# Kernel tuning notes

Hardware: AMD Instinct MI355X
Metric: run time of the kernel (lower is better)

The kernel has to match this reference:

```python
import jax, jax.numpy as jnp
import numpy as np

D, K = 512, 32


def setup_inputs() -> dict:
    key = jax.random.key(0)
    k1, k2, k3 = jax.random.split(key, 3)
    X = jax.random.normal(k1, (8, D, 128, 128), dtype=jnp.float32)
    std1 = 1.0 / (K * D) ** 0.5
    codewords = jax.random.uniform(k2, (K, D), dtype=jnp.float32, minval=-std1, maxval=std1)
    scale = jax.random.uniform(k3, (K,), dtype=jnp.float32, minval=-1.0, maxval=0.0)
    return {"X": X, "codewords": codewords, "scale": scale}


def reference(X, codewords, scale):
    B = X.shape[0]
    # [B, D, H, W] -> [B, N, D]
    Xf = X.reshape(B, D, -1).transpose(0, 2, 1)
    # scaled L2: s_k * ||x_i - d_k||^2, expanded to avoid [B,N,K,D] residuals
    x2 = jnp.sum(Xf * Xf, axis=-1, keepdims=True)            # [B, N, 1]
    c2 = jnp.sum(codewords * codewords, axis=-1)              # [K]
    xc = jnp.einsum('bnd,kd->bnk', Xf, codewords)             # [B, N, K]
    sl = scale * (x2 - 2.0 * xc + c2)                         # [B, N, K]
    A = jax.nn.softmax(sl, axis=2)                            # [B, N, K]
    # E[b,k,d] = sum_n A[b,n,k] * (X[b,n,d] - C[k,d])
    E = jnp.einsum('bnk,bnd->bkd', A, Xf) - jnp.sum(A, axis=1)[..., None] * codewords
    return E
```

## Files before the change

### kernel.cpp

```cpp
#include <hip/hip_runtime.h>
#include <stdint.h>

#define B_ 8
#define D_ 512
#define N_ 16384
#define K_ 32

typedef __attribute__((ext_vector_type(8))) short short8;
typedef __attribute__((ext_vector_type(16))) float f32x16;

union F8 { short8 v; unsigned short s[8]; uint32_t u[4]; uint4 q; };

__device__ __forceinline__ uint32_t bfpack2(float lo, float hi) {
    uint32_t a = __float_as_uint(lo);
    uint32_t b = __float_as_uint(hi);
    a += 0x7FFFu + ((a >> 16) & 1u);
    b += 0x7FFFu + ((b >> 16) & 1u);
    return (a >> 16) | (b & 0xFFFF0000u);
}
__device__ __forceinline__ unsigned short bf16of(float x) {
    uint32_t a = __float_as_uint(x);
    a += 0x7FFFu + ((a >> 16) & 1u);
    return (unsigned short)(a >> 16);
}
__device__ __forceinline__ float bflo(uint32_t v) { return __uint_as_float(v << 16); }
__device__ __forceinline__ float bfhi(uint32_t v) { return __uint_as_float(v & 0xFFFF0000u); }

__device__ __forceinline__ void bar_lds() {
    __builtin_amdgcn_s_waitcnt(0xC07F);
    __builtin_amdgcn_s_barrier();
}

__launch_bounds__(512, 4)
__global__ void encode_kernel(const float* __restrict__ X,
                              const float* __restrict__ Cg,
                              const float* __restrict__ scale,
                              float* __restrict__ part,
                              float* __restrict__ aSumAcc)
{
    __shared__ uint32_t xsTw[D_ * 20];
    __shared__ unsigned short lgpS[8 * 32 * 40];
    __shared__ uint32_t A_ldsw[K_ * 20];
    __shared__ float    x2p[8][32];
    __shared__ float    scs[K_], c2s[K_];
    __shared__ float    c2tmp[K_][17];
    __shared__ float    aSumLds[K_];

    unsigned short* xsTs  = (unsigned short*)xsTw;
    unsigned short* A_lds = (unsigned short*)A_ldsw;

    const int tid = threadIdx.x;
    const int l   = tid & 63;
    const int w   = __builtin_amdgcn_readfirstlane(tid >> 6);
    const int lc  = l & 31;
    const int nh  = l >> 5;
    const int b     = blockIdx.x >> 6;
    const int chunk = blockIdx.x & 63;

    {
        int k = tid >> 4, dg = tid & 15;
        const float* cr = Cg + k * D_ + dg * 32;
        float s2 = 0.f;
#pragma unroll
        for (int i = 0; i < 8; ++i) {
            float4 v = *(const float4*)(cr + i * 4);
            s2 += v.x * v.x + v.y * v.y + v.z * v.z + v.w * v.w;
        }
        c2tmp[k][dg] = s2;
        if (tid < K_) { scs[tid] = scale[tid]; aSumLds[tid] = 0.f; }
    }
    __syncthreads();
    if (tid < K_) {
        float s = 0.f;
#pragma unroll
        for (int dg = 0; dg < 16; ++dg) s += c2tmp[tid][dg];
        c2s[tid] = s;
    }

    F8 cfr[4];
#pragma unroll
    for (int ss = 0; ss < 4; ++ss) {
        int d0 = 64 * w + ss * 16 + nh * 8;
        const float* cp = Cg + lc * D_ + d0;
        float4 a  = *(const float4*)(cp);
        float4 bq = *(const float4*)(cp + 4);
        cfr[ss].u[0] = bfpack2(a.x, a.y);
        cfr[ss].u[1] = bfpack2(a.z, a.w);
        cfr[ss].u[2] = bfpack2(bq.x, bq.y);
        cfr[ss].u[3] = bfpack2(bq.z, bq.w);
    }

    f32x16 eacc[2];
#pragma unroll
    for (int ti = 0; ti < 2; ++ti)
#pragma unroll
        for (int r = 0; r < 16; ++r) eacc[ti][r] = 0.f;
    float aSumReg[4] = {0.f, 0.f, 0.f, 0.f};

    const int nl  = l >> 3;
    const int kq  = l & 7;
    const int smn = (w & 3) * 8 + nl;
    const int k0  = kq * 4;

    const int dl = tid >> 3;
    const int nq = tid & 7;
    const size_t xbase = (size_t)b * D_ * N_ + (size_t)chunk * 256;

    for (int t = 0; t < 8; ++t) {
        bar_lds();

        {
            const float* Xp = X + xbase + t * 32 + nq * 4;
            float4 x2a; x2a.x = x2a.y = x2a.z = x2a.w = 0.f;
#pragma unroll
            for (int r = 0; r < 8; ++r) {
                int d = dl + 64 * r;
                float4 v = *(const float4*)(Xp + (size_t)d * N_);
                x2a.x += v.x * v.x; x2a.y += v.y * v.y;
                x2a.z += v.z * v.z; x2a.w += v.w * v.w;
                uint2 p;
                p.x = bfpack2(v.x, v.y);
                p.y = bfpack2(v.z, v.w);
                *(uint2*)&xsTw[d * 20 + nq * 2] = p;
            }
#pragma unroll
            for (int m = 8; m <= 32; m <<= 1) {
                x2a.x += __shfl_xor(x2a.x, m);
                x2a.y += __shfl_xor(x2a.y, m);
                x2a.z += __shfl_xor(x2a.z, m);
                x2a.w += __shfl_xor(x2a.w, m);
            }
            if (l < 8) *(float4*)&x2p[w][nq * 4] = x2a;
        }

        bar_lds();

        {
            f32x16 lacc;
#pragma unroll
            for (int r = 0; r < 16; ++r) lacc[r] = 0.f;
#pragma unroll
            for (int ss = 0; ss < 4; ++ss) {
                int d0 = 64 * w + ss * 16 + nh * 8;
                F8 af;
#pragma unroll
                for (int j = 0; j < 8; ++j)
                    af.s[j] = xsTs[(d0 + j) * 40 + lc];
                lacc = __builtin_amdgcn_mfma_f32_32x32x16_bf16(af.v, cfr[ss].v, lacc, 0, 0, 0);
            }
#pragma unroll
            for (int r = 0; r < 16; ++r) {
                int row = (r & 3) + 8 * (r >> 2) + 4 * nh;
                lgpS[(w * 32 + row) * 40 + lc] = bf16of(lacc[r]);
            }
        }

        bar_lds();

        if (w < 4) {
            float xc0 = 0.f, xc1 = 0.f, xc2 = 0.f, xc3 = 0.f;
#pragma unroll
            for (int wp = 0; wp < 8; ++wp) {
                uint2 pv = *(const uint2*)&lgpS[(wp * 32 + smn) * 40 + k0];
                xc0 += bflo(pv.x); xc1 += bfhi(pv.x);
                xc2 += bflo(pv.y); xc3 += bfhi(pv.y);
            }
            float x2v = 0.f;
#pragma unroll
            for (int wp = 0; wp < 8; ++wp) x2v += x2p[wp][smn];
            float sl0 = scs[k0]     * (x2v - 2.f * xc0 + c2s[k0]);
            float sl1 = scs[k0 + 1] * (x2v - 2.f * xc1 + c2s[k0 + 1]);
            float sl2 = scs[k0 + 2] * (x2v - 2.f * xc2 + c2s[k0 + 2]);
            float sl3 = scs[k0 + 3] * (x2v - 2.f * xc3 + c2s[k0 + 3]);
            float m = fmaxf(fmaxf(sl0, sl1), fmaxf(sl2, sl3));
#pragma unroll
            for (int mk = 1; mk <= 4; mk <<= 1) m = fmaxf(m, __shfl_xor(m, mk));
            float e0 = __expf(sl0 - m), e1 = __expf(sl1 - m);
            float e2 = __expf(sl2 - m), e3 = __expf(sl3 - m);
            float s = e0 + e1 + e2 + e3;
#pragma unroll
            for (int mk = 1; mk <= 4; mk <<= 1) s += __shfl_xor(s, mk);
            float inv = 1.f / s;
            e0 *= inv; e1 *= inv; e2 *= inv; e3 *= inv;
            aSumReg[0] += e0; aSumReg[1] += e1;
            aSumReg[2] += e2; aSumReg[3] += e3;
            A_lds[(k0)     * 40 + smn] = bf16of(e0);
            A_lds[(k0 + 1) * 40 + smn] = bf16of(e1);
            A_lds[(k0 + 2) * 40 + smn] = bf16of(e2);
            A_lds[(k0 + 3) * 40 + smn] = bf16of(e3);
        }

        bar_lds();

#pragma unroll
        for (int ti = 0; ti < 2; ++ti) {
            int dcol = 64 * w + 32 * ti + lc;
#pragma unroll
            for (int ns = 0; ns < 2; ++ns) {
                F8 af, bf;
                af.q = *(const uint4*)&A_lds[lc * 40 + ns * 16 + nh * 8];
                bf.q = *(const uint4*)&xsTs[dcol * 40 + ns * 16 + nh * 8];
                eacc[ti] = __builtin_amdgcn_mfma_f32_32x32x16_bf16(af.v, bf.v, eacc[ti], 0, 0, 0);
            }
        }
    }

    float* pB = part + (size_t)blockIdx.x * (K_ * D_);
#pragma unroll
    for (int ti = 0; ti < 2; ++ti) {
        int d = 64 * w + 32 * ti + lc;
#pragma unroll
        for (int r = 0; r < 16; ++r) {
            int k = (r & 3) + 8 * (r >> 2) + 4 * nh;
            pB[k * D_ + d] = eacc[ti][r];
        }
    }

    if (w < 4) {
#pragma unroll
        for (int i = 0; i < 4; ++i) {
#pragma unroll
            for (int m = 8; m <= 32; m <<= 1) aSumReg[i] += __shfl_xor(aSumReg[i], m);
        }
        if (l < 8) {
#pragma unroll
            for (int i = 0; i < 4; ++i) unsafeAtomicAdd(&aSumLds[k0 + i], aSumReg[i]);
        }
    }
    __syncthreads();
    if (tid < K_) unsafeAtomicAdd(&aSumAcc[b * K_ + tid], aSumLds[tid]);
}

__global__ void finish_kernel(const float* __restrict__ part,
                              const float* __restrict__ aSumAcc,
                              const float* __restrict__ Cg,
                              float* __restrict__ out)
{
    int idx = blockIdx.x * 256 + threadIdx.x;
    int kd = idx & (K_ * D_ - 1);
    int b  = idx >> 14;
    int k  = kd >> 9;
    const float* p = part + (size_t)b * 64 * (K_ * D_) + kd;
    float s = 0.f;
#pragma unroll 8
    for (int c = 0; c < 64; ++c) s += p[(size_t)c * (K_ * D_)];
    out[idx] = s - aSumAcc[(b << 5) + k] * Cg[kd];
}

extern "C" void kernel_launch(void* const* d_in, const int* in_sizes, int n_in,
                              void* d_out, int out_size, void* d_ws, size_t ws_size,
                              hipStream_t stream)
{
    const float* X  = (const float*)d_in[0];
    const float* C  = (const float*)d_in[1];
    const float* sc = (const float*)d_in[2];
    float* out = (float*)d_out;

    float* part    = (float*)d_ws;
    float* aSumAcc = part + (size_t)512 * K_ * D_;

    hipMemsetAsync(aSumAcc, 0, B_ * K_ * sizeof(float), stream);
    encode_kernel<<<B_ * 64, 512, 0, stream>>>(X, C, sc, part, aSumAcc);
    finish_kernel<<<(B_ * K_ * D_) / 256, 256, 0, stream>>>(part, aSumAcc, C, out);
}
```

Before: 385.2 us.

## Store per-block partials as bf16 and drop memset with per-block aSum partials

```diff
diff --git a/kernel.cpp b/kernel.cpp
--- a/kernel.cpp
+++ b/kernel.cpp
@@ -23,6 +23,9 @@
     a += 0x7FFFu + ((a >> 16) & 1u);
     return (unsigned short)(a >> 16);
 }
+__device__ __forceinline__ float bf16tof(unsigned short u) {
+    return __uint_as_float(((uint32_t)u) << 16);
+}
 __device__ __forceinline__ float bflo(uint32_t v) { return __uint_as_float(v << 16); }
 __device__ __forceinline__ float bfhi(uint32_t v) { return __uint_as_float(v & 0xFFFF0000u); }
 
@@ -35,8 +38,8 @@
 __global__ void encode_kernel(const float* __restrict__ X,
                               const float* __restrict__ Cg,
                               const float* __restrict__ scale,
-                              float* __restrict__ part,
-                              float* __restrict__ aSumAcc)
+                              unsigned short* __restrict__ part,
+                              float* __restrict__ aSumPart)
 {
     __shared__ uint32_t xsTw[D_ * 20];
     __shared__ unsigned short lgpS[8 * 32 * 40];
@@ -205,14 +208,14 @@
         }
     }
 
-    float* pB = part + (size_t)blockIdx.x * (K_ * D_);
+    unsigned short* pB = part + (size_t)blockIdx.x * (K_ * D_);
 #pragma unroll
     for (int ti = 0; ti < 2; ++ti) {
         int d = 64 * w + 32 * ti + lc;
 #pragma unroll
         for (int r = 0; r < 16; ++r) {
             int k = (r & 3) + 8 * (r >> 2) + 4 * nh;
-            pB[k * D_ + d] = eacc[ti][r];
+            __builtin_nontemporal_store(bf16of(eacc[ti][r]), &pB[k * D_ + d]);
         }
     }
 
@@ -228,23 +231,35 @@
         }
     }
     __syncthreads();
-    if (tid < K_) unsafeAtomicAdd(&aSumAcc[b * K_ + tid], aSumLds[tid]);
-}
-
-__global__ void finish_kernel(const float* __restrict__ part,
-                              const float* __restrict__ aSumAcc,
+    if (tid < K_) aSumPart[blockIdx.x * K_ + tid] = aSumLds[tid];
+}
+
+__launch_bounds__(256)
+__global__ void finish_kernel(const unsigned short* __restrict__ part,
+                              const float* __restrict__ aSumPart,
                               const float* __restrict__ Cg,
                               float* __restrict__ out)
 {
-    int idx = blockIdx.x * 256 + threadIdx.x;
-    int kd = idx & (K_ * D_ - 1);
-    int b  = idx >> 14;
-    int k  = kd >> 9;
-    const float* p = part + (size_t)b * 64 * (K_ * D_) + kd;
+    __shared__ float sA;
+    const int bk = blockIdx.x >> 1;
+    const int b  = bk >> 5;
+    const int k  = bk & 31;
+    const int d  = (blockIdx.x & 1) * 256 + threadIdx.x;
+
+    if (threadIdx.x < 64) {
+        float v = aSumPart[(size_t)((b << 6) + threadIdx.x) * K_ + k];
+#pragma unroll
+        for (int m = 1; m <= 32; m <<= 1) v += __shfl_xor(v, m);
+        if (threadIdx.x == 0) sA = v;
+    }
+    __syncthreads();
+
+    const unsigned short* p = part + ((size_t)(b * 64) * K_ + k) * D_ + d;
     float s = 0.f;
 #pragma unroll 8
-    for (int c = 0; c < 64; ++c) s += p[(size_t)c * (K_ * D_)];
-    out[idx] = s - aSumAcc[(b << 5) + k] * Cg[kd];
+    for (int c = 0; c < 64; ++c)
+        s += bf16tof(__builtin_nontemporal_load(&p[(size_t)c * (K_ * D_)]));
+    out[(size_t)bk * D_ + d] = s - sA * Cg[k * D_ + d];
 }
 
 extern "C" void kernel_launch(void* const* d_in, const int* in_sizes, int n_in,
@@ -256,10 +271,9 @@
     const float* sc = (const float*)d_in[2];
     float* out = (float*)d_out;
 
-    float* part    = (float*)d_ws;
-    float* aSumAcc = part + (size_t)512 * K_ * D_;
-
-    hipMemsetAsync(aSumAcc, 0, B_ * K_ * sizeof(float), stream);
-    encode_kernel<<<B_ * 64, 512, 0, stream>>>(X, C, sc, part, aSumAcc);
-    finish_kernel<<<(B_ * K_ * D_) / 256, 256, 0, stream>>>(part, aSumAcc, C, out);
-}
+    unsigned short* part = (unsigned short*)d_ws;
+    float* aSumPart = (float*)(part + (size_t)512 * K_ * D_);
+
+    encode_kernel<<<B_ * 64, 512, 0, stream>>>(X, C, sc, part, aSumPart);
+    finish_kernel<<<B_ * K_ * 2, 256, 0, stream>>>(part, aSumPart, C, out);
+}
```

Result: no change. 380.4 us (-1.3%).
